# Kernel optimization log

Measured on AMD Instinct MI355X. Metric: run time of the kernel, lower is better.

## Reference

```python
import jax, jax.numpy as jnp
import numpy as np
import math

B, T, D, H = 2, 2048, 1024, 16
DH = D // H

def setup_inputs() -> dict:
    key = jax.random.key(0)
    ks = jax.random.split(key, 7)
    s = 0.02
    return {
        "q": jax.random.normal(ks[0], (B, T, D), jnp.float32),
        "k": jax.random.normal(ks[1], (B, T, D), jnp.float32),
        "v": jax.random.normal(ks[2], (B, T, D), jnp.float32),
        "wq": jax.random.normal(ks[3], (D, D), jnp.float32) * s,
        "wk": jax.random.normal(ks[4], (D, D), jnp.float32) * s,
        "wv": jax.random.normal(ks[5], (D, D), jnp.float32) * s,
        "wo": jax.random.normal(ks[6], (D, D), jnp.float32) * s,
    }

def reference(q, k, v, wq, wk, wv, wo):
    # nn.Linear(bias=False): y = x @ W.T
    qh = (q @ wq.T).reshape(B, T, H, DH).transpose(0, 2, 1, 3)  # [B,H,T,DH]
    kh = (k @ wk.T).reshape(B, T, H, DH).transpose(0, 2, 1, 3)
    vh = (v @ wv.T).reshape(B, T, H, DH).transpose(0, 2, 1, 3)
    scores = jnp.einsum('bhqd,bhkd->bhqk', qh, kh) / math.sqrt(DH)
    # causal mask: disallow j > i
    mask = jnp.triu(jnp.ones((T, T), dtype=bool), k=1)
    scores = jnp.where(mask[None, None], -jnp.inf, scores)
    attn = jax.nn.softmax(scores, axis=-1)  # dropout=0 (eval)
    out = jnp.einsum('bhqk,bhkd->bhqd', attn, vh)
    out = out.transpose(0, 2, 1, 3).reshape(B, T, D)
    return out @ wo.T
```

## Files before the change

kernel.cpp:

```cpp
#include <hip/hip_runtime.h>
#include <cstdint>
#include <cstddef>

#define B_  2
#define T_  2048
#define D_  1024
#define H_  16
#define DH_ 64
#define M_  (B_*T_)

typedef __bf16 bf16x8 __attribute__((ext_vector_type(8)));
typedef float  f32x4  __attribute__((ext_vector_type(4)));
typedef unsigned short us4 __attribute__((ext_vector_type(4)));
typedef unsigned short us8 __attribute__((ext_vector_type(8)));
typedef unsigned short ushort_t;

__device__ __forceinline__ unsigned short f32_to_bf16_rne(float f) {
    unsigned u = __builtin_bit_cast(unsigned, f);
    u += 0x7FFFu + ((u >> 16) & 1u);
    return (unsigned short)(u >> 16);
}

__device__ __forceinline__ void async16(const void* g, void* l) {
    __builtin_amdgcn_global_load_lds(
        (const __attribute__((address_space(1))) unsigned int*)(uintptr_t)g,
        (__attribute__((address_space(3))) unsigned int*)(uintptr_t)l, 16, 0, 0);
}

__global__ __launch_bounds__(256) void cvt_all(
    const float* __restrict__ i0, const float* __restrict__ i1, const float* __restrict__ i2,
    const float* __restrict__ i3, const float* __restrict__ i4, const float* __restrict__ i5,
    const float* __restrict__ i6,
    ushort_t* __restrict__ o0, ushort_t* __restrict__ o1, ushort_t* __restrict__ o2,
    ushort_t* __restrict__ o3, ushort_t* __restrict__ o4, ushort_t* __restrict__ o5,
    ushort_t* __restrict__ o6) {
    const int y = blockIdx.y;
    const float* in = y == 0 ? i0 : y == 1 ? i1 : y == 2 ? i2 : y == 3 ? i3
                    : y == 4 ? i4 : y == 5 ? i5 : i6;
    ushort_t* out  = y == 0 ? o0 : y == 1 ? o1 : y == 2 ? o2 : y == 3 ? o3
                    : y == 4 ? o4 : y == 5 ? o5 : o6;
    const int n = (y < 3) ? (M_ * D_) : (D_ * D_);
    int i = (blockIdx.x * 256 + threadIdx.x) * 4;
    if (i >= n) return;
    float4 f = *reinterpret_cast<const float4*>(in + i);
    us4 o;
    o[0] = f32_to_bf16_rne(f.x); o[1] = f32_to_bf16_rne(f.y);
    o[2] = f32_to_bf16_rne(f.z); o[3] = f32_to_bf16_rne(f.w);
    *reinterpret_cast<us4*>(out + i) = o;
}

__device__ __forceinline__ void gemm_mainloop(const ushort_t* __restrict__ A,
                                              const ushort_t* __restrict__ W,
                                              ushort_t* As, ushort_t* Bs,
                                              int m0, int n0, f32x4 acc[4][4]) {
    const int tid  = threadIdx.x;
    const int lc   = tid & 15;
    const int quad = (tid >> 4) & 3;
    const int wave = tid >> 6;
    const int wm = (wave >> 1) * 64, wn = (wave & 1) * 64;
    const int sw = lc & 7;

    const f32x4 fzero = {0.f, 0.f, 0.f, 0.f};
#pragma unroll
    for (int mt = 0; mt < 4; ++mt)
#pragma unroll
        for (int nt = 0; nt < 4; ++nt) acc[mt][nt] = fzero;

    for (int kk = 0; kk < D_; kk += 64) {
        __syncthreads();
#pragma unroll
        for (int i = 0; i < 4; ++i) {
            const int j = i * 256 + tid;
            const int r = j >> 3, c = (j & 7) ^ (r & 7);
            async16(A + (size_t)(m0 + r) * D_ + kk + c * 8, As + j * 8);
            async16(W + (size_t)(n0 + r) * D_ + kk + c * 8, Bs + j * 8);
        }
        __syncthreads();
#pragma unroll
        for (int ks = 0; ks < 2; ++ks) {
            bf16x8 af[4], bw[4];
#pragma unroll
            for (int mt = 0; mt < 4; ++mt)
                af[mt] = *reinterpret_cast<const bf16x8*>(
                    As + (wm + mt * 16 + lc) * 64 + (((ks * 4 + quad) ^ sw) * 8));
#pragma unroll
            for (int nt = 0; nt < 4; ++nt)
                bw[nt] = *reinterpret_cast<const bf16x8*>(
                    Bs + (wn + nt * 16 + lc) * 64 + (((ks * 4 + quad) ^ sw) * 8));
#pragma unroll
            for (int mt = 0; mt < 4; ++mt)
#pragma unroll
                for (int nt = 0; nt < 4; ++nt)
                    acc[mt][nt] = __builtin_amdgcn_mfma_f32_16x16x32_bf16(af[mt], bw[nt], acc[mt][nt], 0, 0, 0);
        }
    }
}

__global__ __launch_bounds__(256, 3) void gemm_qkv(
    const ushort_t* __restrict__ qb, const ushort_t* __restrict__ kb, const ushort_t* __restrict__ vb,
    const ushort_t* __restrict__ wqb, const ushort_t* __restrict__ wkb, const ushort_t* __restrict__ wvb,
    ushort_t* __restrict__ qhb, ushort_t* __restrict__ khb, ushort_t* __restrict__ vtb) {
    __shared__ __align__(16) ushort_t As[128 * 64];
    __shared__ __align__(16) ushort_t Bs[128 * 64];
    __shared__ __align__(16) ushort_t Ts[4][16 * 80];

    const int z = blockIdx.z;
    const ushort_t* A = z == 0 ? qb : z == 1 ? kb : vb;
    const ushort_t* W = z == 0 ? wqb : z == 1 ? wkb : wvb;
    const int yt = blockIdx.x + 8 * (blockIdx.y >> 3);
    const int xt = blockIdx.y & 7;
    const int m0 = yt * 128, n0 = xt * 128;

    f32x4 acc[4][4];
    gemm_mainloop(A, W, As, Bs, m0, n0, acc);

    const int tid = threadIdx.x, lane = tid & 63, lc = tid & 15;
    const int quad = (tid >> 4) & 3, wave = tid >> 6;
    const int wm = (wave >> 1) * 64, wn = (wave & 1) * 64;
    const int mG = m0 + wm;
    const int bb = mG >> 11, t0 = mG & (T_ - 1);
    const int hh = (n0 + wn) >> 6;

    if (z < 2) {
        ushort_t* outp = (z == 0 ? qhb : khb) + ((size_t)bb * H_ + hh) * T_ * DH_;
#pragma unroll
        for (int mt = 0; mt < 4; ++mt) {
#pragma unroll
            for (int nt = 0; nt < 4; ++nt)
#pragma unroll
                for (int r = 0; r < 4; ++r)
                    Ts[wave][(quad * 4 + r) * 80 + nt * 16 + lc] = f32_to_bf16_rne(acc[mt][nt][r]);
#pragma unroll
            for (int it = 0; it < 2; ++it) {
                const int c = it * 64 + lane;
                const int row = c >> 3, c8 = c & 7;
                us8 vv = *reinterpret_cast<const us8*>(Ts[wave] + row * 80 + c8 * 8);
                *reinterpret_cast<us8*>(outp + (size_t)(t0 + mt * 16 + row) * DH_ + c8 * 8) = vv;
            }
        }
    } else {
        ushort_t* base = vtb + ((size_t)bb * H_ + hh) * DH_ * T_;
#pragma unroll
        for (int mt = 0; mt < 4; ++mt) {
#pragma unroll
            for (int nt = 0; nt < 4; ++nt)
#pragma unroll
                for (int r = 0; r < 4; ++r)
                    Ts[wave][(nt * 16 + lc) * 16 + quad * 4 + r] = f32_to_bf16_rne(acc[mt][nt][r]);
#pragma unroll
            for (int it = 0; it < 2; ++it) {
                const int c = it * 64 + lane;
                const int nl = c >> 1, mh = c & 1;
                us8 vv = *reinterpret_cast<const us8*>(Ts[wave] + c * 8);
                *reinterpret_cast<us8*>(base + (size_t)nl * T_ + t0 + mt * 16 + mh * 8) = vv;
            }
        }
    }
}

__global__ __launch_bounds__(256, 4) void gemm_wo(const ushort_t* __restrict__ A,
                                                  const ushort_t* __restrict__ W,
                                                  float* __restrict__ out) {
    __shared__ __align__(16) ushort_t As[64 * 64];
    __shared__ __align__(16) ushort_t Bs[128 * 64];
    const int yt = blockIdx.x + 8 * (blockIdx.y >> 3);
    const int xt = blockIdx.y & 7;
    const int m0 = yt * 64, n0 = xt * 128;

    const int tid = threadIdx.x, lc = tid & 15;
    const int quad = (tid >> 4) & 3, wave = tid >> 6;
    const int wm = (wave >> 1) * 32, wn = (wave & 1) * 64;
    const int sw = lc & 7;

    const f32x4 fzero = {0.f, 0.f, 0.f, 0.f};
    f32x4 acc[2][4];
#pragma unroll
    for (int mt = 0; mt < 2; ++mt)
#pragma unroll
        for (int nt = 0; nt < 4; ++nt) acc[mt][nt] = fzero;

    for (int kk = 0; kk < D_; kk += 64) {
        __syncthreads();
#pragma unroll
        for (int i = 0; i < 2; ++i) {
            const int j = i * 256 + tid;
            const int r = j >> 3, c = (j & 7) ^ (r & 7);
            async16(A + (size_t)(m0 + r) * D_ + kk + c * 8, As + j * 8);
        }
#pragma unroll
        for (int i = 0; i < 4; ++i) {
            const int j = i * 256 + tid;
            const int r = j >> 3, c = (j & 7) ^ (r & 7);
            async16(W + (size_t)(n0 + r) * D_ + kk + c * 8, Bs + j * 8);
        }
        __syncthreads();
#pragma unroll
        for (int ks = 0; ks < 2; ++ks) {
            bf16x8 af[2], bw[4];
#pragma unroll
            for (int mt = 0; mt < 2; ++mt)
                af[mt] = *reinterpret_cast<const bf16x8*>(
                    As + (wm + mt * 16 + lc) * 64 + (((ks * 4 + quad) ^ sw) * 8));
#pragma unroll
            for (int nt = 0; nt < 4; ++nt)
                bw[nt] = *reinterpret_cast<const bf16x8*>(
                    Bs + (wn + nt * 16 + lc) * 64 + (((ks * 4 + quad) ^ sw) * 8));
#pragma unroll
            for (int mt = 0; mt < 2; ++mt)
#pragma unroll
                for (int nt = 0; nt < 4; ++nt)
                    acc[mt][nt] = __builtin_amdgcn_mfma_f32_16x16x32_bf16(af[mt], bw[nt], acc[mt][nt], 0, 0, 0);
        }
    }

#pragma unroll
    for (int mt = 0; mt < 2; ++mt)
#pragma unroll
        for (int nt = 0; nt < 4; ++nt)
#pragma unroll
            for (int r = 0; r < 4; ++r) {
                const int m = m0 + wm + mt * 16 + quad * 4 + r;
                const int n = n0 + wn + nt * 16 + lc;
                out[(size_t)m * D_ + n] = acc[mt][nt][r];
            }
}

__global__ __launch_bounds__(256, 2) void attn4(const ushort_t* __restrict__ Qh,
                                                const ushort_t* __restrict__ Kh,
                                                const ushort_t* __restrict__ Vt,
                                                ushort_t* __restrict__ Ao) {
    __shared__ __align__(16) ushort_t smem[32768 + 4 * 16 * 88];

    const int tid = threadIdx.x, lane = tid & 63, lc = tid & 15;
    const int quad = (tid >> 4) & 3, wave = tid >> 6;
    const int grp = wave >> 1, sub = wave & 1;
    const int sw = lc & 7;

    const int L = blockIdx.x;
    const int xcd = L & 7, slot = L >> 3;
    const int bh = xcd + 8 * (slot >> 4);
    const int xp = slot & 15;
    const int bb = bh >> 4, hh = bh & 15;

    const ushort_t* Qp = Qh + (size_t)bh * T_ * DH_;
    const ushort_t* Kp = Kh + (size_t)bh * T_ * DH_;
    const ushort_t* Vp = Vt + (size_t)bh * DH_ * T_;
    const float SC2 = 0.18033688f;
    const f32x4 fzero = {0.f, 0.f, 0.f, 0.f};

    ushort_t* Pw = smem + 32768 + wave * (16 * 88);

    for (int pass = 0; pass < 2; ++pass) {
        const int qt = pass ? (31 - xp) : xp;
        const int q0 = qt * 64, nkt = qt + 1;
        const int nIt = (nkt + 1) >> 1;
        const int mbase = q0 + sub * 32;

        bf16x8 aq[2][2];
#pragma unroll
        for (int mt = 0; mt < 2; ++mt) {
            const ushort_t* qrow = Qp + (size_t)(mbase + mt * 16 + lc) * DH_ + quad * 8;
            aq[mt][0] = *reinterpret_cast<const bf16x8*>(qrow);
            aq[mt][1] = *reinterpret_cast<const bf16x8*>(qrow + 32);
        }

        f32x4 o[2][4];
        float lsum[2][4];
#pragma unroll
        for (int mt = 0; mt < 2; ++mt) {
#pragma unroll
            for (int ct = 0; ct < 4; ++ct) o[mt][ct] = fzero;
#pragma unroll
            for (int r = 0; r < 4; ++r) lsum[mt][r] = 0.f;
        }

        auto stagePair = [&](int buf, int kt0) {
#pragma unroll
            for (int i = 0; i < 2; ++i) {
                const int j = i * 256 + tid;
                const int r = j >> 3, c = (j & 7) ^ (r & 7);
                const int kprm = 4 * (r & 15) + (r >> 4);
                ushort_t* Kd0 = smem + (buf * 2 + 0) * 4096;
                ushort_t* Kd1 = smem + (buf * 2 + 1) * 4096;
                ushort_t* Vd0 = smem + 16384 + (buf * 2 + 0) * 4096;
                ushort_t* Vd1 = smem + 16384 + (buf * 2 + 1) * 4096;
                if (kt0 < nkt) {
                    async16(Kp + (size_t)(kt0 * 64 + kprm) * DH_ + c * 8, Kd0 + j * 8);
                    async16(Vp + (size_t)r * T_ + kt0 * 64 + c * 8,       Vd0 + j * 8);
                }
                if (kt0 + 1 < nkt) {
                    async16(Kp + (size_t)((kt0 + 1) * 64 + kprm) * DH_ + c * 8, Kd1 + j * 8);
                    async16(Vp + (size_t)r * T_ + (kt0 + 1) * 64 + c * 8,       Vd1 + j * 8);
                }
            }
        };

        __syncthreads();
        stagePair(0, 0);

        for (int it = 0; it < nIt; ++it) {
            const int buf = it & 1;
            __syncthreads();
            if (it + 1 < nIt) stagePair(buf ^ 1, 2 * (it + 1));

            const int kt = 2 * it + grp;
            if (kt < nkt) {
                const int k0 = kt * 64;
                const ushort_t* Kt    = smem + (buf * 2 + grp) * 4096;
                const ushort_t* Vtile = smem + 16384 + (buf * 2 + grp) * 4096;

                bf16x8 bv[4][2];
#pragma unroll
                for (int ct = 0; ct < 4; ++ct) {
                    const ushort_t* vr = Vtile + (ct * 16 + lc) * 64;
                    bv[ct][0] = *reinterpret_cast<const bf16x8*>(vr + ((quad ^ sw) * 8));
                    bv[ct][1] = *reinterpret_cast<const bf16x8*>(vr + (((4 + quad) ^ sw) * 8));
                }

                f32x4 s[2][4];
#pragma unroll
                for (int ct = 0; ct < 4; ++ct) {
                    const ushort_t* kr = Kt + (ct * 16 + lc) * 64;
                    bf16x8 bk0 = *reinterpret_cast<const bf16x8*>(kr + ((quad ^ sw) * 8));
                    bf16x8 bk1 = *reinterpret_cast<const bf16x8*>(kr + (((4 + quad) ^ sw) * 8));
#pragma unroll
                    for (int mt = 0; mt < 2; ++mt) {
                        s[mt][ct] = __builtin_amdgcn_mfma_f32_16x16x32_bf16(aq[mt][0], bk0, fzero, 0, 0, 0);
                        s[mt][ct] = __builtin_amdgcn_mfma_f32_16x16x32_bf16(aq[mt][1], bk1, s[mt][ct], 0, 0, 0);
                    }
                }

#pragma unroll
                for (int mt = 0; mt < 2; ++mt) {
                    float e[4][4];
                    if (kt == qt) {
#pragma unroll
                        for (int ct = 0; ct < 4; ++ct) {
                            const int key = k0 + 4 * lc + ct;
#pragma unroll
                            for (int r = 0; r < 4; ++r) {
                                const int row = mbase + mt * 16 + quad * 4 + r;
                                e[ct][r] = (key <= row) ? __builtin_amdgcn_exp2f(s[mt][ct][r] * SC2) : 0.f;
                            }
                        }
                    } else {
#pragma unroll
                        for (int ct = 0; ct < 4; ++ct)
#pragma unroll
                            for (int r = 0; r < 4; ++r)
                                e[ct][r] = __builtin_amdgcn_exp2f(s[mt][ct][r] * SC2);
                    }
#pragma unroll
                    for (int r = 0; r < 4; ++r) {
                        lsum[mt][r] += e[0][r] + e[1][r] + e[2][r] + e[3][r];
                        us4 pk;
                        pk[0] = f32_to_bf16_rne(e[0][r]); pk[1] = f32_to_bf16_rne(e[1][r]);
                        pk[2] = f32_to_bf16_rne(e[2][r]); pk[3] = f32_to_bf16_rne(e[3][r]);
                        *reinterpret_cast<us4*>(Pw + (quad * 4 + r) * 88 + lc * 4) = pk;
                    }
                    bf16x8 ap0 = *reinterpret_cast<const bf16x8*>(Pw + lc * 88 + quad * 8);
                    bf16x8 ap1 = *reinterpret_cast<const bf16x8*>(Pw + lc * 88 + 32 + quad * 8);
#pragma unroll
                    for (int ct = 0; ct < 4; ++ct) {
                        o[mt][ct] = __builtin_amdgcn_mfma_f32_16x16x32_bf16(ap0, bv[ct][0], o[mt][ct], 0, 0, 0);
                        o[mt][ct] = __builtin_amdgcn_mfma_f32_16x16x32_bf16(ap1, bv[ct][1], o[mt][ct], 0, 0, 0);
                    }
                }
            }
        }

        __syncthreads();
        float* Osh = (float*)smem;
        float* Lsh = (float*)(smem + 16384);
        if (grp == 0) {
#pragma unroll
            for (int mt = 0; mt < 2; ++mt) {
#pragma unroll
                for (int ct = 0; ct < 4; ++ct)
#pragma unroll
                    for (int r = 0; r < 4; ++r)
                        Osh[(sub * 32 + mt * 16 + quad * 4 + r) * 64 + ct * 16 + lc] = o[mt][ct][r];
#pragma unroll
                for (int r = 0; r < 4; ++r)
                    Lsh[(sub * 32 + mt * 16 + quad * 4 + r) * 16 + lc] = lsum[mt][r];
            }
        }
        __syncthreads();
        if (grp == 1) {
#pragma unroll
            for (int mt = 0; mt < 2; ++mt) {
                float inv[4];
#pragma unroll
                for (int r = 0; r < 4; ++r) {
                    float l = lsum[mt][r] + Lsh[(sub * 32 + mt * 16 + quad * 4 + r) * 16 + lc];
#pragma unroll
                    for (int d = 1; d < 16; d <<= 1) l += __shfl_xor(l, d);
                    inv[r] = 1.0f / l;
                }
#pragma unroll
                for (int ct = 0; ct < 4; ++ct)
#pragma unroll
                    for (int r = 0; r < 4; ++r) {
                        const int rowq = mbase + mt * 16 + quad * 4 + r;
                        const float ov = o[mt][ct][r] +
                            Osh[(sub * 32 + mt * 16 + quad * 4 + r) * 64 + ct * 16 + lc];
                        Ao[((size_t)bb * T_ + rowq) * D_ + hh * DH_ + ct * 16 + lc] =
                            f32_to_bf16_rne(ov * inv[r]);
                    }
            }
        }
    }
}

extern "C" void kernel_launch(void* const* d_in, const int* in_sizes, int n_in,
                              void* d_out, int out_size, void* d_ws, size_t ws_size,
                              hipStream_t stream) {
    const float* q  = (const float*)d_in[0];
    const float* k  = (const float*)d_in[1];
    const float* v  = (const float*)d_in[2];
    const float* wq = (const float*)d_in[3];
    const float* wk = (const float*)d_in[4];
    const float* wv = (const float*)d_in[5];
    const float* wo = (const float*)d_in[6];

    char* ws = (char*)d_ws;
    size_t off = 0;
    auto alloc = [&](size_t bytes) -> char* {
        char* p = ws + off;
        off += (bytes + 255) & ~(size_t)255;
        return p;
    };
    ushort_t* qb  = (ushort_t*)alloc((size_t)M_ * D_ * 2);
    ushort_t* kb  = (ushort_t*)alloc((size_t)M_ * D_ * 2);
    ushort_t* vb  = (ushort_t*)alloc((size_t)M_ * D_ * 2);
    ushort_t* wqb = (ushort_t*)alloc((size_t)D_ * D_ * 2);
    ushort_t* wkb = (ushort_t*)alloc((size_t)D_ * D_ * 2);
    ushort_t* wvb = (ushort_t*)alloc((size_t)D_ * D_ * 2);
    ushort_t* wob = (ushort_t*)alloc((size_t)D_ * D_ * 2);
    ushort_t* qhb = (ushort_t*)alloc((size_t)M_ * D_ * 2);
    ushort_t* khb = (ushort_t*)alloc((size_t)M_ * D_ * 2);
    ushort_t* vtb = (ushort_t*)alloc((size_t)M_ * D_ * 2);
    ushort_t* aob = (ushort_t*)alloc((size_t)M_ * D_ * 2);

    cvt_all<<<dim3(4096, 7), 256, 0, stream>>>(q, k, v, wq, wk, wv, wo,
                                               qb, kb, vb, wqb, wkb, wvb, wob);

    gemm_qkv<<<dim3(8, 32, 3), 256, 0, stream>>>(qb, kb, vb, wqb, wkb, wvb, qhb, khb, vtb);

    attn4<<<dim3(512), 256, 0, stream>>>(qhb, khb, vtb, aob);

    gemm_wo<<<dim3(8, 64), 256, 0, stream>>>(aob, wob, (float*)d_out);
}
```

Measured before the change: 197.9 us.

## Rewrite attention as register-streamed kernel without LDS staging or split-K merge

The attention kernel is restructured: each 128-thread block handles one 64-row query tile (longest tiles first) instead of pairing two tiles with a 4-wave split-K over keys. K and V fragments are loaded straight from global memory into registers, double-buffering K in registers, instead of async-staging into LDS with block-wide barriers, and the cross-group partial-output merge through shared memory is removed. The bf16 conversion uses a cheaper add-and-byte-permute packing, which rounds ties away from zero instead of to even. This removes barriers and LDS traffic and raises block count, but K/V now come from L2/global without reuse across waves and register pressure rises.

Measured after the change: 273.6 us. 1.38x slower.

```diff
diff --git a/kernel.cpp b/kernel.cpp
--- a/kernel.cpp
+++ b/kernel.cpp
@@ -19,6 +19,12 @@
     unsigned u = __builtin_bit_cast(unsigned, f);
     u += 0x7FFFu + ((u >> 16) & 1u);
     return (unsigned short)(u >> 16);
+}
+
+__device__ __forceinline__ unsigned pack_bf16_2(float f0, float f1) {
+    unsigned a = __builtin_bit_cast(unsigned, f0) + 0x8000u;
+    unsigned b = __builtin_bit_cast(unsigned, f1) + 0x8000u;
+    return __builtin_amdgcn_perm(b, a, 0x07060302u);
 }
 
 __device__ __forceinline__ void async16(const void* g, void* l) {
@@ -43,10 +49,10 @@
     int i = (blockIdx.x * 256 + threadIdx.x) * 4;
     if (i >= n) return;
     float4 f = *reinterpret_cast<const float4*>(in + i);
-    us4 o;
-    o[0] = f32_to_bf16_rne(f.x); o[1] = f32_to_bf16_rne(f.y);
-    o[2] = f32_to_bf16_rne(f.z); o[3] = f32_to_bf16_rne(f.w);
-    *reinterpret_cast<us4*>(out + i) = o;
+    unsigned lo = pack_bf16_2(f.x, f.y);
+    unsigned hi = pack_bf16_2(f.z, f.w);
+    *reinterpret_cast<unsigned long long*>(out + i) =
+        (unsigned long long)lo | ((unsigned long long)hi << 32);
 }
 
 __device__ __forceinline__ void gemm_mainloop(const ushort_t* __restrict__ A,
@@ -225,190 +231,154 @@
             }
 }
 
-__global__ __launch_bounds__(256, 2) void attn4(const ushort_t* __restrict__ Qh,
+__global__ __launch_bounds__(128, 2) void attn5(const ushort_t* __restrict__ Qh,
                                                 const ushort_t* __restrict__ Kh,
                                                 const ushort_t* __restrict__ Vt,
                                                 ushort_t* __restrict__ Ao) {
-    __shared__ __align__(16) ushort_t smem[32768 + 4 * 16 * 88];
-
-    const int tid = threadIdx.x, lane = tid & 63, lc = tid & 15;
+    __shared__ __align__(16) ushort_t Ps[2][16 * 88];
+
+    const int tid = threadIdx.x, lc = tid & 15;
     const int quad = (tid >> 4) & 3, wave = tid >> 6;
-    const int grp = wave >> 1, sub = wave & 1;
-    const int sw = lc & 7;
 
     const int L = blockIdx.x;
-    const int xcd = L & 7, slot = L >> 3;
-    const int bh = xcd + 8 * (slot >> 4);
-    const int xp = slot & 15;
+    const int xcd = L & 7, s = L >> 3;
+    const int bh = xcd + 8 * (s >> 5);
+    const int qt = 31 - (s & 31);
     const int bb = bh >> 4, hh = bh & 15;
+    const int q0 = qt * 64, nkt = qt + 1;
+    const int mbase = q0 + wave * 32;
 
     const ushort_t* Qp = Qh + (size_t)bh * T_ * DH_;
     const ushort_t* Kp = Kh + (size_t)bh * T_ * DH_;
     const ushort_t* Vp = Vt + (size_t)bh * DH_ * T_;
     const float SC2 = 0.18033688f;
     const f32x4 fzero = {0.f, 0.f, 0.f, 0.f};
-
-    ushort_t* Pw = smem + 32768 + wave * (16 * 88);
-
-    for (int pass = 0; pass < 2; ++pass) {
-        const int qt = pass ? (31 - xp) : xp;
-        const int q0 = qt * 64, nkt = qt + 1;
-        const int nIt = (nkt + 1) >> 1;
-        const int mbase = q0 + sub * 32;
-
-        bf16x8 aq[2][2];
+    ushort_t* Pw = Ps[wave];
+
+    bf16x8 aq[2][2];
+#pragma unroll
+    for (int mt = 0; mt < 2; ++mt) {
+        const ushort_t* qrow = Qp + (size_t)(mbase + mt * 16 + lc) * DH_ + quad * 8;
+        aq[mt][0] = *reinterpret_cast<const bf16x8*>(qrow);
+        aq[mt][1] = *reinterpret_cast<const bf16x8*>(qrow + 32);
+    }
+
+    f32x4 o[2][4];
+    float lsum[2][4];
+#pragma unroll
+    for (int mt = 0; mt < 2; ++mt) {
+#pragma unroll
+        for (int ct = 0; ct < 4; ++ct) o[mt][ct] = fzero;
+#pragma unroll
+        for (int r = 0; r < 4; ++r) lsum[mt][r] = 0.f;
+    }
+
+    bf16x8 bkA[4][2], bkB[4][2], bv[4][2];
+
+    auto loadK = [&](int kt, bf16x8 (&bk)[4][2]) {
+#pragma unroll
+        for (int ct = 0; ct < 4; ++ct) {
+            const ushort_t* kr = Kp + (size_t)(kt * 64 + 4 * lc + ct) * DH_ + quad * 8;
+            bk[ct][0] = *reinterpret_cast<const bf16x8*>(kr);
+            bk[ct][1] = *reinterpret_cast<const bf16x8*>(kr + 32);
+        }
+    };
+    auto loadV = [&](int kt) {
+#pragma unroll
+        for (int ct = 0; ct < 4; ++ct) {
+            const ushort_t* vr = Vp + (size_t)(ct * 16 + lc) * T_ + kt * 64 + quad * 8;
+            bv[ct][0] = *reinterpret_cast<const bf16x8*>(vr);
+            bv[ct][1] = *reinterpret_cast<const bf16x8*>(vr + 32);
+        }
+    };
+    auto computeS = [&](bf16x8 (&bk)[4][2], f32x4 (&sc)[2][4]) {
+#pragma unroll
+        for (int ct = 0; ct < 4; ++ct)
+#pragma unroll
+            for (int mt = 0; mt < 2; ++mt) {
+                sc[mt][ct] = __builtin_amdgcn_mfma_f32_16x16x32_bf16(aq[mt][0], bk[ct][0], fzero, 0, 0, 0);
+                sc[mt][ct] = __builtin_amdgcn_mfma_f32_16x16x32_bf16(aq[mt][1], bk[ct][1], sc[mt][ct], 0, 0, 0);
+            }
+    };
+    auto softmaxPV = [&](int kt, f32x4 (&sc)[2][4]) {
+        const int k0 = kt * 64;
 #pragma unroll
         for (int mt = 0; mt < 2; ++mt) {
-            const ushort_t* qrow = Qp + (size_t)(mbase + mt * 16 + lc) * DH_ + quad * 8;
-            aq[mt][0] = *reinterpret_cast<const bf16x8*>(qrow);
-            aq[mt][1] = *reinterpret_cast<const bf16x8*>(qrow + 32);
-        }
-
-        f32x4 o[2][4];
-        float lsum[2][4];
-#pragma unroll
-        for (int mt = 0; mt < 2; ++mt) {
-#pragma unroll
-            for (int ct = 0; ct < 4; ++ct) o[mt][ct] = fzero;
-#pragma unroll
-            for (int r = 0; r < 4; ++r) lsum[mt][r] = 0.f;
-        }
-
-        auto stagePair = [&](int buf, int kt0) {
-#pragma unroll
-            for (int i = 0; i < 2; ++i) {
-                const int j = i * 256 + tid;
-                const int r = j >> 3, c = (j & 7) ^ (r & 7);
-                const int kprm = 4 * (r & 15) + (r >> 4);
-                ushort_t* Kd0 = smem + (buf * 2 + 0) * 4096;
-                ushort_t* Kd1 = smem + (buf * 2 + 1) * 4096;
-                ushort_t* Vd0 = smem + 16384 + (buf * 2 + 0) * 4096;
-                ushort_t* Vd1 = smem + 16384 + (buf * 2 + 1) * 4096;
-                if (kt0 < nkt) {
-                    async16(Kp + (size_t)(kt0 * 64 + kprm) * DH_ + c * 8, Kd0 + j * 8);
-                    async16(Vp + (size_t)r * T_ + kt0 * 64 + c * 8,       Vd0 + j * 8);
-                }
-                if (kt0 + 1 < nkt) {
-                    async16(Kp + (size_t)((kt0 + 1) * 64 + kprm) * DH_ + c * 8, Kd1 + j * 8);
-                    async16(Vp + (size_t)r * T_ + (kt0 + 1) * 64 + c * 8,       Vd1 + j * 8);
-                }
-            }
-        };
-
-        __syncthreads();
-        stagePair(0, 0);
-
-        for (int it = 0; it < nIt; ++it) {
-            const int buf = it & 1;
-            __syncthreads();
-            if (it + 1 < nIt) stagePair(buf ^ 1, 2 * (it + 1));
-
-            const int kt = 2 * it + grp;
-            if (kt < nkt) {
-                const int k0 = kt * 64;
-                const ushort_t* Kt    = smem + (buf * 2 + grp) * 4096;
-                const ushort_t* Vtile = smem + 16384 + (buf * 2 + grp) * 4096;
-
-                bf16x8 bv[4][2];
+            float e[4][4];
+            if (kt == qt) {
 #pragma unroll
                 for (int ct = 0; ct < 4; ++ct) {
-                    const ushort_t* vr = Vtile + (ct * 16 + lc) * 64;
-                    bv[ct][0] = *reinterpret_cast<const bf16x8*>(vr + ((quad ^ sw) * 8));
-                    bv[ct][1] = *reinterpret_cast<const bf16x8*>(vr + (((4 + quad) ^ sw) * 8));
-                }
-
-                f32x4 s[2][4];
-#pragma unroll
-                for (int ct = 0; ct < 4; ++ct) {
-                    const ushort_t* kr = Kt + (ct * 16 + lc) * 64;
-                    bf16x8 bk0 = *reinterpret_cast<const bf16x8*>(kr + ((quad ^ sw) * 8));
-                    bf16x8 bk1 = *reinterpret_cast<const bf16x8*>(kr + (((4 + quad) ^ sw) * 8));
-#pragma unroll
-                    for (int mt = 0; mt < 2; ++mt) {
-                        s[mt][ct] = __builtin_amdgcn_mfma_f32_16x16x32_bf16(aq[mt][0], bk0, fzero, 0, 0, 0);
-                        s[mt][ct] = __builtin_amdgcn_mfma_f32_16x16x32_bf16(aq[mt][1], bk1, s[mt][ct], 0, 0, 0);
+                    const int key = k0 + 4 * lc + ct;
+#pragma unroll
+                    for (int r = 0; r < 4; ++r) {
+                        const int row = mbase + mt * 16 + quad * 4 + r;
+                        e[ct][r] = (key <= row) ? __builtin_amdgcn_exp2f(sc[mt][ct][r] * SC2) : 0.f;
                     }
                 }
-
-#pragma unroll
-                for (int mt = 0; mt < 2; ++mt) {
-                    float e[4][4];
-                    if (kt == qt) {
-#pragma unroll
-                        for (int ct = 0; ct < 4; ++ct) {
-                            const int key = k0 + 4 * lc + ct;
-#pragma unroll
-                            for (int r = 0; r < 4; ++r) {
-                                const int row = mbase + mt * 16 + quad * 4 + r;
-                                e[ct][r] = (key <= row) ? __builtin_amdgcn_exp2f(s[mt][ct][r] * SC2) : 0.f;
-                            }
-                        }
-                    } else {
-#pragma unroll
-                        for (int ct = 0; ct < 4; ++ct)
-#pragma unroll
-                            for (int r = 0; r < 4; ++r)
-                                e[ct][r] = __builtin_amdgcn_exp2f(s[mt][ct][r] * SC2);
-                    }
-#pragma unroll
-                    for (int r = 0; r < 4; ++r) {
-                        lsum[mt][r] += e[0][r] + e[1][r] + e[2][r] + e[3][r];
-                        us4 pk;
-                        pk[0] = f32_to_bf16_rne(e[0][r]); pk[1] = f32_to_bf16_rne(e[1][r]);
-                        pk[2] = f32_to_bf16_rne(e[2][r]); pk[3] = f32_to_bf16_rne(e[3][r]);
-                        *reinterpret_cast<us4*>(Pw + (quad * 4 + r) * 88 + lc * 4) = pk;
-                    }
-                    bf16x8 ap0 = *reinterpret_cast<const bf16x8*>(Pw + lc * 88 + quad * 8);
-                    bf16x8 ap1 = *reinterpret_cast<const bf16x8*>(Pw + lc * 88 + 32 + quad * 8);
-#pragma unroll
-                    for (int ct = 0; ct < 4; ++ct) {
-                        o[mt][ct] = __builtin_amdgcn_mfma_f32_16x16x32_bf16(ap0, bv[ct][0], o[mt][ct], 0, 0, 0);
-                        o[mt][ct] = __builtin_amdgcn_mfma_f32_16x16x32_bf16(ap1, bv[ct][1], o[mt][ct], 0, 0, 0);
-                    }
-                }
-            }
-        }
-
-        __syncthreads();
-        float* Osh = (float*)smem;
-        float* Lsh = (float*)(smem + 16384);
-        if (grp == 0) {
-#pragma unroll
-            for (int mt = 0; mt < 2; ++mt) {
+            } else {
 #pragma unroll
                 for (int ct = 0; ct < 4; ++ct)
 #pragma unroll
                     for (int r = 0; r < 4; ++r)
-                        Osh[(sub * 32 + mt * 16 + quad * 4 + r) * 64 + ct * 16 + lc] = o[mt][ct][r];
-#pragma unroll
-                for (int r = 0; r < 4; ++r)
-                    Lsh[(sub * 32 + mt * 16 + quad * 4 + r) * 16 + lc] = lsum[mt][r];
-            }
-        }
-        __syncthreads();
-        if (grp == 1) {
-#pragma unroll
-            for (int mt = 0; mt < 2; ++mt) {
-                float inv[4];
-#pragma unroll
-                for (int r = 0; r < 4; ++r) {
-                    float l = lsum[mt][r] + Lsh[(sub * 32 + mt * 16 + quad * 4 + r) * 16 + lc];
-#pragma unroll
-                    for (int d = 1; d < 16; d <<= 1) l += __shfl_xor(l, d);
-                    inv[r] = 1.0f / l;
-                }
-#pragma unroll
-                for (int ct = 0; ct < 4; ++ct)
-#pragma unroll
-                    for (int r = 0; r < 4; ++r) {
-                        const int rowq = mbase + mt * 16 + quad * 4 + r;
-                        const float ov = o[mt][ct][r] +
-                            Osh[(sub * 32 + mt * 16 + quad * 4 + r) * 64 + ct * 16 + lc];
-                        Ao[((size_t)bb * T_ + rowq) * D_ + hh * DH_ + ct * 16 + lc] =
-                            f32_to_bf16_rne(ov * inv[r]);
-                    }
-            }
-        }
+                        e[ct][r] = __builtin_amdgcn_exp2f(sc[mt][ct][r] * SC2);
+            }
+#pragma unroll
+            for (int r = 0; r < 4; ++r) {
+                lsum[mt][r] += (e[0][r] + e[1][r]) + (e[2][r] + e[3][r]);
+                unsigned lo = pack_bf16_2(e[0][r], e[1][r]);
+                unsigned hi = pack_bf16_2(e[2][r], e[3][r]);
+                *reinterpret_cast<unsigned long long*>(Pw + (quad * 4 + r) * 88 + lc * 4) =
+                    (unsigned long long)lo | ((unsigned long long)hi << 32);
+            }
+            bf16x8 ap0 = *reinterpret_cast<const bf16x8*>(Pw + lc * 88 + quad * 8);
+            bf16x8 ap1 = *reinterpret_cast<const bf16x8*>(Pw + lc * 88 + 32 + quad * 8);
+#pragma unroll
+            for (int ct = 0; ct < 4; ++ct) {
+                o[mt][ct] = __builtin_amdgcn_mfma_f32_16x16x32_bf16(ap0, bv[ct][0], o[mt][ct], 0, 0, 0);
+                o[mt][ct] = __builtin_amdgcn_mfma_f32_16x16x32_bf16(ap1, bv[ct][1], o[mt][ct], 0, 0, 0);
+            }
+        }
+    };
+
+    loadK(0, bkA);
+    int kt = 0;
+    while (true) {
+        {
+            loadV(kt);
+            f32x4 sc[2][4];
+            computeS(bkA, sc);
+            if (kt + 1 < nkt) loadK(kt + 1, bkB);
+            softmaxPV(kt, sc);
+        }
+        if (++kt >= nkt) break;
+        {
+            loadV(kt);
+            f32x4 sc[2][4];
+            computeS(bkB, sc);
+            if (kt + 1 < nkt) loadK(kt + 1, bkA);
+            softmaxPV(kt, sc);
+        }
+        if (++kt >= nkt) break;
+    }
+
+#pragma unroll
+    for (int mt = 0; mt < 2; ++mt) {
+        float inv[4];
+#pragma unroll
+        for (int r = 0; r < 4; ++r) {
+            float l = lsum[mt][r];
+#pragma unroll
+            for (int d = 1; d < 16; d <<= 1) l += __shfl_xor(l, d);
+            inv[r] = 1.0f / l;
+        }
+#pragma unroll
+        for (int ct = 0; ct < 4; ++ct)
+#pragma unroll
+            for (int r = 0; r < 4; ++r) {
+                const int row = mbase + mt * 16 + quad * 4 + r;
+                Ao[((size_t)bb * T_ + row) * D_ + hh * DH_ + ct * 16 + lc] =
+                    f32_to_bf16_rne(o[mt][ct][r] * inv[r]);
+            }
     }
 }
 
@@ -447,7 +417,7 @@
 
     gemm_qkv<<<dim3(8, 32, 3), 256, 0, stream>>>(qb, kb, vb, wqb, wkb, wvb, qhb, khb, vtb);
 
-    attn4<<<dim3(512), 256, 0, stream>>>(qhb, khb, vtb, aob);
+    attn5<<<dim3(1024), 128, 0, stream>>>(qhb, khb, vtb, aob);
 
     gemm_wo<<<dim3(8, 64), 256, 0, stream>>>(aob, wob, (float*)d_out);
 }
```

## Split attention into one q-tile per block with single-buffer LDS for occupancy

Applied to the files above, without the earlier changes.

The attention kernel previously processed two paired q-tiles per block with double-buffered K/V staging. It now launches 1024 blocks, one q-tile each and heaviest first, and drops the double buffer to halve LDS so three blocks fit per CU. The price is that K/V loads are no longer overlapped with compute within a block, which relies on other resident blocks to hide latency. It also replaces per-element bf16 rounding with a cheaper add-and-perm packing (round-half-up rather than ties-to-even) in both the conversion kernel and the P store, and shrinks the P row padding.

After: 187.3 us. 1.06x faster.

```diff
diff --git a/kernel.cpp b/kernel.cpp
--- a/kernel.cpp
+++ b/kernel.cpp
@@ -19,6 +19,12 @@
     unsigned u = __builtin_bit_cast(unsigned, f);
     u += 0x7FFFu + ((u >> 16) & 1u);
     return (unsigned short)(u >> 16);
+}
+
+__device__ __forceinline__ unsigned pack_bf16_2(float f0, float f1) {
+    unsigned a = __builtin_bit_cast(unsigned, f0) + 0x8000u;
+    unsigned b = __builtin_bit_cast(unsigned, f1) + 0x8000u;
+    return __builtin_amdgcn_perm(b, a, 0x07060302u);
 }
 
 __device__ __forceinline__ void async16(const void* g, void* l) {
@@ -43,10 +49,10 @@
     int i = (blockIdx.x * 256 + threadIdx.x) * 4;
     if (i >= n) return;
     float4 f = *reinterpret_cast<const float4*>(in + i);
-    us4 o;
-    o[0] = f32_to_bf16_rne(f.x); o[1] = f32_to_bf16_rne(f.y);
-    o[2] = f32_to_bf16_rne(f.z); o[3] = f32_to_bf16_rne(f.w);
-    *reinterpret_cast<us4*>(out + i) = o;
+    unsigned lo = pack_bf16_2(f.x, f.y);
+    unsigned hi = pack_bf16_2(f.z, f.w);
+    *reinterpret_cast<unsigned long long*>(out + i) =
+        (unsigned long long)lo | ((unsigned long long)hi << 32);
 }
 
 __device__ __forceinline__ void gemm_mainloop(const ushort_t* __restrict__ A,
@@ -225,11 +231,11 @@
             }
 }
 
-__global__ __launch_bounds__(256, 2) void attn4(const ushort_t* __restrict__ Qh,
+__global__ __launch_bounds__(256, 3) void attn6(const ushort_t* __restrict__ Qh,
                                                 const ushort_t* __restrict__ Kh,
                                                 const ushort_t* __restrict__ Vt,
                                                 ushort_t* __restrict__ Ao) {
-    __shared__ __align__(16) ushort_t smem[32768 + 4 * 16 * 88];
+    __shared__ __align__(16) ushort_t smem[16384 + 4 * 16 * 72];
 
     const int tid = threadIdx.x, lane = tid & 63, lc = tid & 15;
     const int quad = (tid >> 4) & 3, wave = tid >> 6;
@@ -237,177 +243,160 @@
     const int sw = lc & 7;
 
     const int L = blockIdx.x;
-    const int xcd = L & 7, slot = L >> 3;
-    const int bh = xcd + 8 * (slot >> 4);
-    const int xp = slot & 15;
+    const int xcd = L & 7, s = L >> 3;
+    const int qt = 31 - (s >> 2);
+    const int bh = xcd + 8 * (s & 3);
     const int bb = bh >> 4, hh = bh & 15;
+    const int q0 = qt * 64, nkt = qt + 1;
+    const int nIt = (nkt + 1) >> 1;
+    const int mbase = q0 + sub * 32;
 
     const ushort_t* Qp = Qh + (size_t)bh * T_ * DH_;
     const ushort_t* Kp = Kh + (size_t)bh * T_ * DH_;
     const ushort_t* Vp = Vt + (size_t)bh * DH_ * T_;
     const float SC2 = 0.18033688f;
     const f32x4 fzero = {0.f, 0.f, 0.f, 0.f};
-
-    ushort_t* Pw = smem + 32768 + wave * (16 * 88);
-
-    for (int pass = 0; pass < 2; ++pass) {
-        const int qt = pass ? (31 - xp) : xp;
-        const int q0 = qt * 64, nkt = qt + 1;
-        const int nIt = (nkt + 1) >> 1;
-        const int mbase = q0 + sub * 32;
-
-        bf16x8 aq[2][2];
+    ushort_t* Pw = smem + 16384 + wave * (16 * 72);
+
+    bf16x8 aq[2][2];
+#pragma unroll
+    for (int mt = 0; mt < 2; ++mt) {
+        const ushort_t* qrow = Qp + (size_t)(mbase + mt * 16 + lc) * DH_ + quad * 8;
+        aq[mt][0] = *reinterpret_cast<const bf16x8*>(qrow);
+        aq[mt][1] = *reinterpret_cast<const bf16x8*>(qrow + 32);
+    }
+
+    f32x4 o[2][4];
+    float lsum[2][4];
+#pragma unroll
+    for (int mt = 0; mt < 2; ++mt) {
+#pragma unroll
+        for (int ct = 0; ct < 4; ++ct) o[mt][ct] = fzero;
+#pragma unroll
+        for (int r = 0; r < 4; ++r) lsum[mt][r] = 0.f;
+    }
+
+    for (int it = 0; it < nIt; ++it) {
+        const int kt0 = 2 * it;
+        __syncthreads();
+#pragma unroll
+        for (int i = 0; i < 2; ++i) {
+            const int j = i * 256 + tid;
+            const int r = j >> 3, c = (j & 7) ^ (r & 7);
+            const int kprm = 4 * (r & 15) + (r >> 4);
+            async16(Kp + (size_t)(kt0 * 64 + kprm) * DH_ + c * 8, smem + j * 8);
+            async16(Vp + (size_t)r * T_ + kt0 * 64 + c * 8,       smem + 8192 + j * 8);
+            if (kt0 + 1 < nkt) {
+                async16(Kp + (size_t)((kt0 + 1) * 64 + kprm) * DH_ + c * 8, smem + 4096 + j * 8);
+                async16(Vp + (size_t)r * T_ + (kt0 + 1) * 64 + c * 8,       smem + 12288 + j * 8);
+            }
+        }
+        __syncthreads();
+
+        const int kt = kt0 + grp;
+        if (kt < nkt) {
+            const int k0 = kt * 64;
+            const ushort_t* Kt    = smem + grp * 4096;
+            const ushort_t* Vtile = smem + 8192 + grp * 4096;
+
+            bf16x8 bv[4][2];
+#pragma unroll
+            for (int ct = 0; ct < 4; ++ct) {
+                const ushort_t* vr = Vtile + (ct * 16 + lc) * 64;
+                bv[ct][0] = *reinterpret_cast<const bf16x8*>(vr + ((quad ^ sw) * 8));
+                bv[ct][1] = *reinterpret_cast<const bf16x8*>(vr + (((4 + quad) ^ sw) * 8));
+            }
+
+            f32x4 sc[2][4];
+#pragma unroll
+            for (int ct = 0; ct < 4; ++ct) {
+                const ushort_t* kr = Kt + (ct * 16 + lc) * 64;
+                bf16x8 bk0 = *reinterpret_cast<const bf16x8*>(kr + ((quad ^ sw) * 8));
+                bf16x8 bk1 = *reinterpret_cast<const bf16x8*>(kr + (((4 + quad) ^ sw) * 8));
+#pragma unroll
+                for (int mt = 0; mt < 2; ++mt) {
+                    sc[mt][ct] = __builtin_amdgcn_mfma_f32_16x16x32_bf16(aq[mt][0], bk0, fzero, 0, 0, 0);
+                    sc[mt][ct] = __builtin_amdgcn_mfma_f32_16x16x32_bf16(aq[mt][1], bk1, sc[mt][ct], 0, 0, 0);
+                }
+            }
+
+#pragma unroll
+            for (int mt = 0; mt < 2; ++mt) {
+                float e[4][4];
+                if (kt == qt) {
+#pragma unroll
+                    for (int ct = 0; ct < 4; ++ct) {
+                        const int key = k0 + 4 * lc + ct;
+#pragma unroll
+                        for (int r = 0; r < 4; ++r) {
+                            const int row = mbase + mt * 16 + quad * 4 + r;
+                            e[ct][r] = (key <= row) ? __builtin_amdgcn_exp2f(sc[mt][ct][r] * SC2) : 0.f;
+                        }
+                    }
+                } else {
+#pragma unroll
+                    for (int ct = 0; ct < 4; ++ct)
+#pragma unroll
+                        for (int r = 0; r < 4; ++r)
+                            e[ct][r] = __builtin_amdgcn_exp2f(sc[mt][ct][r] * SC2);
+                }
+#pragma unroll
+                for (int r = 0; r < 4; ++r) {
+                    lsum[mt][r] += (e[0][r] + e[1][r]) + (e[2][r] + e[3][r]);
+                    unsigned lo = pack_bf16_2(e[0][r], e[1][r]);
+                    unsigned hi = pack_bf16_2(e[2][r], e[3][r]);
+                    *reinterpret_cast<unsigned long long*>(Pw + (quad * 4 + r) * 72 + lc * 4) =
+                        (unsigned long long)lo | ((unsigned long long)hi << 32);
+                }
+                bf16x8 ap0 = *reinterpret_cast<const bf16x8*>(Pw + lc * 72 + quad * 8);
+                bf16x8 ap1 = *reinterpret_cast<const bf16x8*>(Pw + lc * 72 + 32 + quad * 8);
+#pragma unroll
+                for (int ct = 0; ct < 4; ++ct) {
+                    o[mt][ct] = __builtin_amdgcn_mfma_f32_16x16x32_bf16(ap0, bv[ct][0], o[mt][ct], 0, 0, 0);
+                    o[mt][ct] = __builtin_amdgcn_mfma_f32_16x16x32_bf16(ap1, bv[ct][1], o[mt][ct], 0, 0, 0);
+                }
+            }
+        }
+    }
+
+    __syncthreads();
+    float* Osh = (float*)smem;
+    float* Lsh = (float*)(smem + 8192);
+    if (grp == 0) {
 #pragma unroll
         for (int mt = 0; mt < 2; ++mt) {
-            const ushort_t* qrow = Qp + (size_t)(mbase + mt * 16 + lc) * DH_ + quad * 8;
-            aq[mt][0] = *reinterpret_cast<const bf16x8*>(qrow);
-            aq[mt][1] = *reinterpret_cast<const bf16x8*>(qrow + 32);
-        }
-
-        f32x4 o[2][4];
-        float lsum[2][4];
+#pragma unroll
+            for (int ct = 0; ct < 4; ++ct)
+#pragma unroll
+                for (int r = 0; r < 4; ++r)
+                    Osh[(sub * 32 + mt * 16 + quad * 4 + r) * 64 + ct * 16 + lc] = o[mt][ct][r];
+#pragma unroll
+            for (int r = 0; r < 4; ++r)
+                Lsh[(sub * 32 + mt * 16 + quad * 4 + r) * 16 + lc] = lsum[mt][r];
+        }
+    }
+    __syncthreads();
+    if (grp == 1) {
 #pragma unroll
         for (int mt = 0; mt < 2; ++mt) {
-#pragma unroll
-            for (int ct = 0; ct < 4; ++ct) o[mt][ct] = fzero;
-#pragma unroll
-            for (int r = 0; r < 4; ++r) lsum[mt][r] = 0.f;
-        }
-
-        auto stagePair = [&](int buf, int kt0) {
-#pragma unroll
-            for (int i = 0; i < 2; ++i) {
-                const int j = i * 256 + tid;
-                const int r = j >> 3, c = (j & 7) ^ (r & 7);
-                const int kprm = 4 * (r & 15) + (r >> 4);
-                ushort_t* Kd0 = smem + (buf * 2 + 0) * 4096;
-                ushort_t* Kd1 = smem + (buf * 2 + 1) * 4096;
-                ushort_t* Vd0 = smem + 16384 + (buf * 2 + 0) * 4096;
-                ushort_t* Vd1 = smem + 16384 + (buf * 2 + 1) * 4096;
-                if (kt0 < nkt) {
-                    async16(Kp + (size_t)(kt0 * 64 + kprm) * DH_ + c * 8, Kd0 + j * 8);
-                    async16(Vp + (size_t)r * T_ + kt0 * 64 + c * 8,       Vd0 + j * 8);
+            float inv[4];
+#pragma unroll
+            for (int r = 0; r < 4; ++r) {
+                float l = lsum[mt][r] + Lsh[(sub * 32 + mt * 16 + quad * 4 + r) * 16 + lc];
+#pragma unroll
+                for (int d = 1; d < 16; d <<= 1) l += __shfl_xor(l, d);
+                inv[r] = 1.0f / l;
+            }
+#pragma unroll
+            for (int ct = 0; ct < 4; ++ct)
+#pragma unroll
+                for (int r = 0; r < 4; ++r) {
+                    const int rowq = mbase + mt * 16 + quad * 4 + r;
+                    const float ov = o[mt][ct][r] +
+                        Osh[(sub * 32 + mt * 16 + quad * 4 + r) * 64 + ct * 16 + lc];
+                    Ao[((size_t)bb * T_ + rowq) * D_ + hh * DH_ + ct * 16 + lc] =
+                        f32_to_bf16_rne(ov * inv[r]);
                 }
-                if (kt0 + 1 < nkt) {
-                    async16(Kp + (size_t)((kt0 + 1) * 64 + kprm) * DH_ + c * 8, Kd1 + j * 8);
-                    async16(Vp + (size_t)r * T_ + (kt0 + 1) * 64 + c * 8,       Vd1 + j * 8);
-                }
-            }
-        };
-
-        __syncthreads();
-        stagePair(0, 0);
-
-        for (int it = 0; it < nIt; ++it) {
-            const int buf = it & 1;
-            __syncthreads();
-            if (it + 1 < nIt) stagePair(buf ^ 1, 2 * (it + 1));
-
-            const int kt = 2 * it + grp;
-            if (kt < nkt) {
-                const int k0 = kt * 64;
-                const ushort_t* Kt    = smem + (buf * 2 + grp) * 4096;
-                const ushort_t* Vtile = smem + 16384 + (buf * 2 + grp) * 4096;
-
-                bf16x8 bv[4][2];
-#pragma unroll
-                for (int ct = 0; ct < 4; ++ct) {
-                    const ushort_t* vr = Vtile + (ct * 16 + lc) * 64;
-                    bv[ct][0] = *reinterpret_cast<const bf16x8*>(vr + ((quad ^ sw) * 8));
-                    bv[ct][1] = *reinterpret_cast<const bf16x8*>(vr + (((4 + quad) ^ sw) * 8));
-                }
-
-                f32x4 s[2][4];
-#pragma unroll
-                for (int ct = 0; ct < 4; ++ct) {
-                    const ushort_t* kr = Kt + (ct * 16 + lc) * 64;
-                    bf16x8 bk0 = *reinterpret_cast<const bf16x8*>(kr + ((quad ^ sw) * 8));
-                    bf16x8 bk1 = *reinterpret_cast<const bf16x8*>(kr + (((4 + quad) ^ sw) * 8));
-#pragma unroll
-                    for (int mt = 0; mt < 2; ++mt) {
-                        s[mt][ct] = __builtin_amdgcn_mfma_f32_16x16x32_bf16(aq[mt][0], bk0, fzero, 0, 0, 0);
-                        s[mt][ct] = __builtin_amdgcn_mfma_f32_16x16x32_bf16(aq[mt][1], bk1, s[mt][ct], 0, 0, 0);
-                    }
-                }
-
-#pragma unroll
-                for (int mt = 0; mt < 2; ++mt) {
-                    float e[4][4];
-                    if (kt == qt) {
-#pragma unroll
-                        for (int ct = 0; ct < 4; ++ct) {
-                            const int key = k0 + 4 * lc + ct;
-#pragma unroll
-                            for (int r = 0; r < 4; ++r) {
-                                const int row = mbase + mt * 16 + quad * 4 + r;
-                                e[ct][r] = (key <= row) ? __builtin_amdgcn_exp2f(s[mt][ct][r] * SC2) : 0.f;
-                            }
-                        }
-                    } else {
-#pragma unroll
-                        for (int ct = 0; ct < 4; ++ct)
-#pragma unroll
-                            for (int r = 0; r < 4; ++r)
-                                e[ct][r] = __builtin_amdgcn_exp2f(s[mt][ct][r] * SC2);
-                    }
-#pragma unroll
-                    for (int r = 0; r < 4; ++r) {
-                        lsum[mt][r] += e[0][r] + e[1][r] + e[2][r] + e[3][r];
-                        us4 pk;
-                        pk[0] = f32_to_bf16_rne(e[0][r]); pk[1] = f32_to_bf16_rne(e[1][r]);
-                        pk[2] = f32_to_bf16_rne(e[2][r]); pk[3] = f32_to_bf16_rne(e[3][r]);
-                        *reinterpret_cast<us4*>(Pw + (quad * 4 + r) * 88 + lc * 4) = pk;
-                    }
-                    bf16x8 ap0 = *reinterpret_cast<const bf16x8*>(Pw + lc * 88 + quad * 8);
-                    bf16x8 ap1 = *reinterpret_cast<const bf16x8*>(Pw + lc * 88 + 32 + quad * 8);
-#pragma unroll
-                    for (int ct = 0; ct < 4; ++ct) {
-                        o[mt][ct] = __builtin_amdgcn_mfma_f32_16x16x32_bf16(ap0, bv[ct][0], o[mt][ct], 0, 0, 0);
-                        o[mt][ct] = __builtin_amdgcn_mfma_f32_16x16x32_bf16(ap1, bv[ct][1], o[mt][ct], 0, 0, 0);
-                    }
-                }
-            }
-        }
-
-        __syncthreads();
-        float* Osh = (float*)smem;
-        float* Lsh = (float*)(smem + 16384);
-        if (grp == 0) {
-#pragma unroll
-            for (int mt = 0; mt < 2; ++mt) {
-#pragma unroll
-                for (int ct = 0; ct < 4; ++ct)
-#pragma unroll
-                    for (int r = 0; r < 4; ++r)
-                        Osh[(sub * 32 + mt * 16 + quad * 4 + r) * 64 + ct * 16 + lc] = o[mt][ct][r];
-#pragma unroll
-                for (int r = 0; r < 4; ++r)
-                    Lsh[(sub * 32 + mt * 16 + quad * 4 + r) * 16 + lc] = lsum[mt][r];
-            }
-        }
-        __syncthreads();
-        if (grp == 1) {
-#pragma unroll
-            for (int mt = 0; mt < 2; ++mt) {
-                float inv[4];
-#pragma unroll
-                for (int r = 0; r < 4; ++r) {
-                    float l = lsum[mt][r] + Lsh[(sub * 32 + mt * 16 + quad * 4 + r) * 16 + lc];
-#pragma unroll
-                    for (int d = 1; d < 16; d <<= 1) l += __shfl_xor(l, d);
-                    inv[r] = 1.0f / l;
-                }
-#pragma unroll
-                for (int ct = 0; ct < 4; ++ct)
-#pragma unroll
-                    for (int r = 0; r < 4; ++r) {
-                        const int rowq = mbase + mt * 16 + quad * 4 + r;
-                        const float ov = o[mt][ct][r] +
-                            Osh[(sub * 32 + mt * 16 + quad * 4 + r) * 64 + ct * 16 + lc];
-                        Ao[((size_t)bb * T_ + rowq) * D_ + hh * DH_ + ct * 16 + lc] =
-                            f32_to_bf16_rne(ov * inv[r]);
-                    }
-            }
         }
     }
 }
@@ -447,7 +436,7 @@
 
     gemm_qkv<<<dim3(8, 32, 3), 256, 0, stream>>>(qb, kb, vb, wqb, wkb, wvb, qhb, khb, vtb);
 
-    attn4<<<dim3(512), 256, 0, stream>>>(qhb, khb, vtb, aob);
+    attn6<<<dim3(1024), 256, 0, stream>>>(qhb, khb, vtb, aob);
 
     gemm_wo<<<dim3(8, 64), 256, 0, stream>>>(aob, wob, (float*)d_out);
 }
```
